# Optimization experiments

Hardware: AMD Instinct MI355X
Metric: run time of the kernel (lower is better)

## Reference

```python
import jax, jax.numpy as jnp
import numpy as np


def setup_inputs() -> dict:
    key = jax.random.key(0)
    k1, k2, k3, k4 = jax.random.split(key, 4)
    n_nodes, n_edges, d_in, d_half = 100000, 1600000, 256, 128
    x = jax.random.normal(k1, (n_nodes, d_in), dtype=jnp.float32)
    edge_index = jax.random.randint(k2, (2, n_edges), 0, n_nodes, dtype=jnp.int64)
    W_f = jax.random.normal(k3, (d_half, d_in), dtype=jnp.float32) * (1.0 / np.sqrt(d_in))
    W_b = jax.random.normal(k4, (d_half, d_in), dtype=jnp.float32) * (1.0 / np.sqrt(d_in))
    bias_param = jnp.zeros((2 * d_half,), dtype=jnp.float32)
    return {"x": x, "edge_index": edge_index, "W_f": W_f, "W_b": W_b, "bias_param": bias_param}


def _inv_sqrt(deg):
    # deg.pow(-0.5) with inf -> 0
    return jnp.where(deg > 0, jax.lax.rsqrt(deg), 0.0)


def reference(x, edge_index, W_f, W_b, bias_param):
    n_nodes = x.shape[0]
    # add_remaining_self_loops with fill value 1
    loops = jnp.arange(n_nodes, dtype=edge_index.dtype)
    ei = jnp.concatenate([edge_index, jnp.stack([loops, loops])], axis=1)
    n_e = ei.shape[1]
    w = jnp.ones((n_e,), dtype=x.dtype)
    # directed_norm, flow='source_to_target': col, row = edge_index
    col, row = ei[0], ei[1]
    in_deg = jax.ops.segment_sum(w, col, num_segments=n_nodes)
    out_deg = jax.ops.segment_sum(w, row, num_segments=n_nodes)
    ew = _inv_sqrt(out_deg)[row] * w * _inv_sqrt(in_deg)[col]  # [E]
    # adj_forward: source=row, target=col ; adj_backward: source=col, target=row
    mf = (x @ W_f.T)[row] * ew[:, None]           # [E, d_half]
    y_forward = jax.ops.segment_sum(mf, col, num_segments=n_nodes)
    mb = (x @ W_b.T)[col] * ew[:, None]           # [E, d_half]
    y_backward = jax.ops.segment_sum(mb, row, num_segments=n_nodes)
    y = jnp.concatenate([y_forward, y_backward], axis=-1) + bias_param
    return y
```

## Files before the change

### kernel.cpp

```cpp
#include <hip/hip_runtime.h>

#define D_IN 256
#define D_HALF 128

typedef __attribute__((ext_vector_type(8))) short short8;
typedef __attribute__((ext_vector_type(4))) float float4v;

__device__ __forceinline__ unsigned short f2bf(float f) {
    union { float f; unsigned u; } v; v.f = f;
    unsigned r = v.u + 0x7FFF + ((v.u >> 16) & 1);
    return (unsigned short)(r >> 16);
}
__device__ __forceinline__ float bflo(unsigned u) { union { unsigned u; float f; } v; v.u = u << 16; return v.f; }
__device__ __forceinline__ float bfhi(unsigned u) { union { unsigned u; float f; } v; v.u = u & 0xffff0000u; return v.f; }

__device__ __forceinline__ void async16(const void* g, void* l) {
    __builtin_amdgcn_global_load_lds(
        (const __attribute__((address_space(1))) unsigned int*)g,
        (__attribute__((address_space(3))) unsigned int*)l, 16, 0, 0);
}


#define S_SH 9
#define NBK_MAX 512
#define CAP 12288
#define EPB 4096

__global__ void zero_kernel(int* __restrict__ gcnt) {
    int i = blockIdx.x * blockDim.x + threadIdx.x;
    if (i < NBK_MAX) gcnt[i] = 0;
}

__global__ void p1_kernel(const int* __restrict__ col, const int* __restrict__ row,
                          int* __restrict__ gcnt, unsigned* __restrict__ staging,
                          int N, int E) {
    __shared__ int hist[NBK_MAX];
    __shared__ int base_[NBK_MAX];
    const int tid = threadIdx.x;
    hist[tid] = 0; hist[tid + 256] = 0;
    __syncthreads();

    int ce[16], re[16], rf_[16], rb_[16];
    const int e0 = blockIdx.x * EPB;
    #pragma unroll
    for (int j = 0; j < 16; ++j) {
        int e = e0 + j * 256 + tid;
        if (e < E) {
            ce[j] = col[e];
            re[j] = row[e];
            rf_[j] = atomicAdd(&hist[ce[j] >> S_SH], 1);
            rb_[j] = atomicAdd(&hist[(N + re[j]) >> S_SH], 1);
        } else {
            ce[j] = -1; re[j] = 0; rf_[j] = 0; rb_[j] = 0;
        }
    }
    __syncthreads();

    #pragma unroll
    for (int b = 0; b < NBK_MAX / 256; ++b) {
        int idx = b * 256 + tid;
        int c = hist[idx];
        if (c) base_[idx] = idx * CAP + atomicAdd(&gcnt[idx], c);
    }
    __syncthreads();

    #pragma unroll
    for (int j = 0; j < 16; ++j) {
        if (ce[j] >= 0) {
            int c = ce[j], r = re[j];
            staging[(size_t)base_[c >> S_SH] + rf_[j]] =
                ((unsigned)(c & 511) << 23) | (unsigned)r;
            int sb = N + r;
            staging[(size_t)base_[sb >> S_SH] + rb_[j]] =
                ((unsigned)(sb & 511) << 23) | (unsigned)c;
        }
    }
}

__global__ void scanB_kernel(const int* __restrict__ gcnt, int* __restrict__ bbase, int nbuck) {
    __shared__ int s[NBK_MAX];
    const int tid = threadIdx.x;
    int v = (tid < nbuck) ? gcnt[tid] : 0;
    s[tid] = v;
    __syncthreads();
    for (int d = 1; d < NBK_MAX; d <<= 1) {
        int t = (tid >= d) ? s[tid - d] : 0;
        __syncthreads();
        s[tid] += t;
        __syncthreads();
    }
    if (tid < nbuck) bbase[tid] = s[tid] - v;
}

__global__ void bsort_kernel(const unsigned* __restrict__ staging, const int* __restrict__ gcnt,
                             const int* __restrict__ bbase, int* __restrict__ cnt,
                             int* __restrict__ offs, int* __restrict__ adj, int M) {
    __shared__ int lcnt[NBK_MAX];
    __shared__ int s[256];
    __shared__ int lbuf[CAP];
    const int tid = threadIdx.x;
    const int b = blockIdx.x;
    const int s0 = b << S_SH;
    lcnt[tid] = 0; lcnt[tid + 256] = 0;
    __syncthreads();

    const int count = gcnt[b];
    const int base = bbase[b];
    const unsigned* __restrict__ st = staging + (size_t)b * CAP;

    for (int i = tid; i < count; i += 256)
        atomicAdd(&lcnt[st[i] >> 23], 1);
    __syncthreads();

    int v0 = lcnt[2 * tid], v1 = lcnt[2 * tid + 1];
    int pair = v0 + v1;
    s[tid] = pair;
    __syncthreads();
    for (int d = 1; d < 256; d <<= 1) {
        int t = (tid >= d) ? s[tid - d] : 0;
        __syncthreads();
        s[tid] += t;
        __syncthreads();
    }
    int excl = s[tid] - pair;

    int gs0 = s0 + 2 * tid;
    if (gs0 < M)     { cnt[gs0] = v0;     offs[gs0] = base + excl; }
    if (gs0 + 1 < M) { cnt[gs0 + 1] = v1; offs[gs0 + 1] = base + excl + v0; }

    lcnt[2 * tid] = excl;
    lcnt[2 * tid + 1] = excl + v0;
    __syncthreads();

    for (int i = tid; i < count; i += 256) {
        unsigned it = st[i];
        int sl = it >> 23;
        int p = atomicAdd(&lcnt[sl], 1);
        lbuf[p] = (int)(it & 0x7fffffu);
    }
    __syncthreads();
    for (int i = tid; i < count; i += 256)
        adj[base + i] = lbuf[i];
}

__global__ void inv_kernel(const int* __restrict__ cnt,
                           float* __restrict__ inv_in, float* __restrict__ inv_out, int N) {
    int i = blockIdx.x * blockDim.x + threadIdx.x;
    if (i < N) {
        inv_in[i]  = rsqrtf((float)(cnt[i] + 1));
        inv_out[i] = rsqrtf((float)(cnt[N + i] + 1));
    }
}


__global__ void cast_kernel(const float* __restrict__ x, const float* __restrict__ Wf,
                            const float* __restrict__ Wb, unsigned short* __restrict__ xb,
                            unsigned short* __restrict__ wcat, int n4) {
    int i = blockIdx.x * blockDim.x + threadIdx.x;
    const int w4 = (2 * D_HALF * D_IN) / 4;
    if (i < n4) {
        float4 v = ((const float4*)x)[i];
        ushort4 o = { f2bf(v.x), f2bf(v.y), f2bf(v.z), f2bf(v.w) };
        ((ushort4*)xb)[i] = o;
    } else if (i < n4 + w4) {
        int j = i - n4;
        int elem = j * 4;
        const float* src = (elem < D_HALF * D_IN) ? (Wf + elem) : (Wb + (elem - D_HALF * D_IN));
        float4 v = *(const float4*)src;
        ushort4 o = { f2bf(v.x), f2bf(v.y), f2bf(v.z), f2bf(v.w) };
        ((ushort4*)wcat)[j] = o;
    }
}


#define BM 128
#define BN 128
#define BK 32

__global__ void gemm_mfma_kernel(const unsigned short* __restrict__ xb,
                                 const unsigned short* __restrict__ wcat,
                                 const float* __restrict__ inv_in,
                                 const float* __restrict__ inv_out,
                                 unsigned short* __restrict__ zb, int N) {
    __shared__ __align__(16) unsigned short As[BM * BK];
    __shared__ __align__(16) unsigned short Bs[BN * BK];
    const int tid = threadIdx.x;
    const int wave = tid >> 6;
    const int lane = tid & 63;
    const int bm = blockIdx.x * BM;
    const int bn = blockIdx.y * BN;
    const int warpM = wave >> 1;
    const int warpN = wave & 1;
    const int l15 = lane & 15;
    const int quad = lane >> 4;

    float4v acc[4][4];
    #pragma unroll
    for (int i = 0; i < 4; ++i)
        #pragma unroll
        for (int j = 0; j < 4; ++j)
            acc[i][j] = (float4v){0.f, 0.f, 0.f, 0.f};

    for (int kt = 0; kt < D_IN / BK; ++kt) {
        #pragma unroll
        for (int iss = 0; iss < 2; ++iss) {
            const int pbase = iss * 256 + wave * 64;
            const int p = pbase + lane;
            const int m = p >> 2;
            const int g = (p & 3) ^ ((m >> 1) & 3);
            int gm = bm + m; if (gm >= N) gm = N - 1;
            async16(xb + (size_t)gm * D_IN + kt * BK + g * 8, &As[pbase * 8]);
            async16(wcat + (size_t)(bn + m) * D_IN + kt * BK + g * 8, &Bs[pbase * 8]);
        }
        __syncthreads();

        short8 af[4], bfr[4];
        #pragma unroll
        for (int mi = 0; mi < 4; ++mi) {
            int m = warpM * 64 + mi * 16 + l15;
            af[mi] = *(const short8*)&As[m * BK + (quad ^ ((m >> 1) & 3)) * 8];
        }
        #pragma unroll
        for (int ni = 0; ni < 4; ++ni) {
            int n = warpN * 64 + ni * 16 + l15;
            bfr[ni] = *(const short8*)&Bs[n * BK + (quad ^ ((n >> 1) & 3)) * 8];
        }
        #pragma unroll
        for (int mi = 0; mi < 4; ++mi)
            #pragma unroll
            for (int ni = 0; ni < 4; ++ni)
                acc[mi][ni] = __builtin_amdgcn_mfma_f32_16x16x32_bf16(af[mi], bfr[ni], acc[mi][ni], 0, 0, 0);
        __syncthreads();
    }

    const float* __restrict__ sc = (blockIdx.y == 0) ? inv_out : inv_in;
    #pragma unroll
    for (int mi = 0; mi < 4; ++mi) {
        #pragma unroll
        for (int reg = 0; reg < 4; ++reg) {
            int gm = bm + warpM * 64 + mi * 16 + quad * 4 + reg;
            if (gm < N) {
                float s = sc[gm];
                #pragma unroll
                for (int ni = 0; ni < 4; ++ni) {
                    int gn = bn + warpN * 64 + ni * 16 + l15;
                    zb[(size_t)gm * D_IN + gn] = f2bf(acc[mi][ni][reg] * s);
                }
            }
        }
    }
}


__global__ void gather_kernel(const unsigned short* __restrict__ zb, const int* __restrict__ adj,
                              const int* __restrict__ offs, const int* __restrict__ cnt,
                              const float* __restrict__ inv_in, const float* __restrict__ inv_out,
                              const float* __restrict__ bias,
                              float* __restrict__ out, int N) {
    const int wave = threadIdx.x >> 6;
    const int lane = threadIdx.x & 63;
    const int slot = blockIdx.x * 4 + wave;
    if (slot >= 2 * N) return;
    const int dir = (slot >= N) ? 1 : 0;
    const int node = slot - dir * N;
    const int csr = slot;
    const int beg = offs[csr];
    const int deg = cnt[csr];
    const int end = beg + deg;
    const int g4 = lane >> 4;
    const int l15 = lane & 15;
    const int chu = dir * D_HALF + 8 * l15;
    const int pa = g4 << 2;

    float a0 = 0.f, a1 = 0.f, a2 = 0.f, a3 = 0.f;
    float a4 = 0.f, a5 = 0.f, a6 = 0.f, a7 = 0.f;

    for (int base = beg; base < end; base += 64) {
        int len = end - base; if (len > 64) len = 64;
        int nb = (lane < len) ? adj[base + lane] : node;
        #pragma unroll 8
        for (int j0 = 0; j0 < len; j0 += 4) {
            int nsel = __builtin_amdgcn_ds_bpermute((j0 << 2) + pa, nb);
            float m = (j0 + g4 < len) ? 1.0f : 0.0f;
            const uint4 u = *(const uint4*)&zb[(size_t)nsel * D_IN + chu];
            a0 = fmaf(m, bflo(u.x), a0); a1 = fmaf(m, bfhi(u.x), a1);
            a2 = fmaf(m, bflo(u.y), a2); a3 = fmaf(m, bfhi(u.y), a3);
            a4 = fmaf(m, bflo(u.z), a4); a5 = fmaf(m, bfhi(u.z), a5);
            a6 = fmaf(m, bflo(u.w), a6); a7 = fmaf(m, bfhi(u.w), a7);
        }
    }

    a0 += __shfl_xor(a0, 16); a0 += __shfl_xor(a0, 32);
    a1 += __shfl_xor(a1, 16); a1 += __shfl_xor(a1, 32);
    a2 += __shfl_xor(a2, 16); a2 += __shfl_xor(a2, 32);
    a3 += __shfl_xor(a3, 16); a3 += __shfl_xor(a3, 32);
    a4 += __shfl_xor(a4, 16); a4 += __shfl_xor(a4, 32);
    a5 += __shfl_xor(a5, 16); a5 += __shfl_xor(a5, 32);
    a6 += __shfl_xor(a6, 16); a6 += __shfl_xor(a6, 32);
    a7 += __shfl_xor(a7, 16); a7 += __shfl_xor(a7, 32);

    if (g4 == 0) {
        const uint4 us = *(const uint4*)&zb[(size_t)node * D_IN + chu];
        a0 += bflo(us.x); a1 += bfhi(us.x);
        a2 += bflo(us.y); a3 += bfhi(us.y);
        a4 += bflo(us.z); a5 += bfhi(us.z);
        a6 += bflo(us.w); a7 += bfhi(us.w);

        const float scale = dir ? inv_out[node] : inv_in[node];
        const float4 bv0 = *(const float4*)&bias[chu];
        const float4 bv1 = *(const float4*)&bias[chu + 4];
        size_t oi = (size_t)node * D_IN + chu;
        float4 o0 = { bv0.x + scale * a0, bv0.y + scale * a1,
                      bv0.z + scale * a2, bv0.w + scale * a3 };
        float4 o1 = { bv1.x + scale * a4, bv1.y + scale * a5,
                      bv1.z + scale * a6, bv1.w + scale * a7 };
        *(float4*)&out[oi] = o0;
        *(float4*)&out[oi + 4] = o1;
    }
}


extern "C" void kernel_launch(void* const* d_in, const int* in_sizes, int n_in,
                              void* d_out, int out_size, void* d_ws, size_t ws_size,
                              hipStream_t stream) {
    const float* x    = (const float*)d_in[0];
    const int*   ei   = (const int*)d_in[1];
    const float* Wf   = (const float*)d_in[2];
    const float* Wb   = (const float*)d_in[3];
    const float* bias = (const float*)d_in[4];
    float* out = (float*)d_out;

    const int N = in_sizes[0] / D_IN;
    const int E = in_sizes[1] / 2;
    const int* col = ei;
    const int* rowp = ei + E;

    char* ws = (char*)d_ws;
    unsigned short* xb = (unsigned short*)ws;   ws += (size_t)N * D_IN * sizeof(short);
    unsigned short* zb = (unsigned short*)ws;   ws += (size_t)N * D_IN * sizeof(short);
    unsigned short* wcat = (unsigned short*)ws; ws += (size_t)2 * D_HALF * D_IN * sizeof(short);
    int* cnt = (int*)ws;            ws += (size_t)2 * N * sizeof(int);
    int* offs = (int*)ws;           ws += (size_t)2 * N * sizeof(int);
    float* inv_in = (float*)ws;     ws += (size_t)N * sizeof(float);
    float* inv_out = (float*)ws;    ws += (size_t)N * sizeof(float);
    int* adj = (int*)ws;            ws += (size_t)2 * E * sizeof(int);
    int* gcnt = (int*)ws;           ws += NBK_MAX * sizeof(int);
    int* bbase = (int*)ws;          ws += NBK_MAX * sizeof(int);

    unsigned* staging = (unsigned*)zb;

    const int M = 2 * N;
    const int nbuck = (M + 511) >> S_SH;

    const int n4 = N * D_IN / 4;
    const int w4 = (2 * D_HALF * D_IN) / 4;
    cast_kernel<<<(n4 + w4 + 255) / 256, 256, 0, stream>>>(x, Wf, Wb, xb, wcat, n4);

    zero_kernel<<<2, 256, 0, stream>>>(gcnt);
    p1_kernel<<<(E + EPB - 1) / EPB, 256, 0, stream>>>(col, rowp, gcnt, staging, N, E);
    scanB_kernel<<<1, NBK_MAX, 0, stream>>>(gcnt, bbase, nbuck);
    bsort_kernel<<<nbuck, 256, 0, stream>>>(staging, gcnt, bbase, cnt, offs, adj, M);
    inv_kernel<<<(N + 255) / 256, 256, 0, stream>>>(cnt, inv_in, inv_out, N);

    dim3 ggrid((N + BM - 1) / BM, D_IN / BN);
    gemm_mfma_kernel<<<ggrid, 256, 0, stream>>>(xb, wcat, inv_in, inv_out, zb, N);

    gather_kernel<<<(2 * N + 3) / 4, 256, 0, stream>>>(zb, adj, offs, cnt, inv_in, inv_out, bias, out, N);
}
```

Measured before the change: 394.9 us.

## Fuse cast into edge-bucketing kernel and fold scan and rsqrt into bucket sort

The bf16 cast of x and weights now runs as extra blocks of the edge-bucketing kernel, so the two independent jobs share one launch and can overlap. The global bucket-offset scan moves into every bucket-sort block, each of which redundantly scans all bucket counts. The inverse-sqrt degree computation is also done inside the bucket sort. This removes three launches and their serialization at the cost of redundant per-block scan work. gcnt is read for indices up to 511, which is fine since zero_kernel clears all 512 entries.

```diff
diff --git a/kernel.cpp b/kernel.cpp
--- a/kernel.cpp
+++ b/kernel.cpp
@@ -31,12 +31,34 @@
     if (i < NBK_MAX) gcnt[i] = 0;
 }
 
-__global__ void p1_kernel(const int* __restrict__ col, const int* __restrict__ row,
-                          int* __restrict__ gcnt, unsigned* __restrict__ staging,
-                          int N, int E) {
+__global__ void p1_cast_kernel(const int* __restrict__ col, const int* __restrict__ row,
+                               int* __restrict__ gcnt, unsigned* __restrict__ staging,
+                               int N, int E, int nP1,
+                               const float* __restrict__ x, const float* __restrict__ Wf,
+                               const float* __restrict__ Wb, unsigned short* __restrict__ xb,
+                               unsigned short* __restrict__ wcat, int n4) {
     __shared__ int hist[NBK_MAX];
     __shared__ int base_[NBK_MAX];
     const int tid = threadIdx.x;
+
+    if (blockIdx.x >= nP1) {
+        int i = (blockIdx.x - nP1) * 256 + tid;
+        const int w4 = (2 * D_HALF * D_IN) / 4;
+        if (i < n4) {
+            float4 v = ((const float4*)x)[i];
+            ushort4 o = { f2bf(v.x), f2bf(v.y), f2bf(v.z), f2bf(v.w) };
+            ((ushort4*)xb)[i] = o;
+        } else if (i < n4 + w4) {
+            int j = i - n4;
+            int elem = j * 4;
+            const float* src = (elem < D_HALF * D_IN) ? (Wf + elem) : (Wb + (elem - D_HALF * D_IN));
+            float4 v = *(const float4*)src;
+            ushort4 o = { f2bf(v.x), f2bf(v.y), f2bf(v.z), f2bf(v.w) };
+            ((ushort4*)wcat)[j] = o;
+        }
+        return;
+    }
+
     hist[tid] = 0; hist[tid + 256] = 0;
     __syncthreads();
 
@@ -77,35 +99,38 @@
     }
 }
 
-__global__ void scanB_kernel(const int* __restrict__ gcnt, int* __restrict__ bbase, int nbuck) {
-    __shared__ int s[NBK_MAX];
-    const int tid = threadIdx.x;
-    int v = (tid < nbuck) ? gcnt[tid] : 0;
-    s[tid] = v;
-    __syncthreads();
-    for (int d = 1; d < NBK_MAX; d <<= 1) {
-        int t = (tid >= d) ? s[tid - d] : 0;
-        __syncthreads();
-        s[tid] += t;
-        __syncthreads();
-    }
-    if (tid < nbuck) bbase[tid] = s[tid] - v;
-}
-
 __global__ void bsort_kernel(const unsigned* __restrict__ staging, const int* __restrict__ gcnt,
-                             const int* __restrict__ bbase, int* __restrict__ cnt,
-                             int* __restrict__ offs, int* __restrict__ adj, int M) {
+                             int* __restrict__ cnt, int* __restrict__ offs,
+                             float* __restrict__ inv_in, float* __restrict__ inv_out,
+                             int* __restrict__ adj, int N, int M) {
     __shared__ int lcnt[NBK_MAX];
     __shared__ int s[256];
     __shared__ int lbuf[CAP];
+    __shared__ int bc[2];
     const int tid = threadIdx.x;
     const int b = blockIdx.x;
     const int s0 = b << S_SH;
+
+    int g0 = gcnt[2 * tid], g1 = gcnt[2 * tid + 1];
+    int pairB = g0 + g1;
+    s[tid] = pairB;
+    __syncthreads();
+    for (int d = 1; d < 256; d <<= 1) {
+        int t = (tid >= d) ? s[tid - d] : 0;
+        __syncthreads();
+        s[tid] += t;
+        __syncthreads();
+    }
+    if (tid == (b >> 1)) {
+        int excl = s[tid] - pairB;
+        bc[0] = excl + ((b & 1) ? g0 : 0);
+        bc[1] = (b & 1) ? g1 : g0;
+    }
     lcnt[tid] = 0; lcnt[tid + 256] = 0;
     __syncthreads();
 
-    const int count = gcnt[b];
-    const int base = bbase[b];
+    const int base = bc[0];
+    const int count = bc[1];
     const unsigned* __restrict__ st = staging + (size_t)b * CAP;
 
     for (int i = tid; i < count; i += 256)
@@ -125,8 +150,16 @@
     int excl = s[tid] - pair;
 
     int gs0 = s0 + 2 * tid;
-    if (gs0 < M)     { cnt[gs0] = v0;     offs[gs0] = base + excl; }
-    if (gs0 + 1 < M) { cnt[gs0 + 1] = v1; offs[gs0 + 1] = base + excl + v0; }
+    if (gs0 < M) {
+        cnt[gs0] = v0;  offs[gs0] = base + excl;
+        if (gs0 < N) inv_in[gs0] = rsqrtf((float)(v0 + 1));
+        else         inv_out[gs0 - N] = rsqrtf((float)(v0 + 1));
+    }
+    if (gs0 + 1 < M) {
+        cnt[gs0 + 1] = v1;  offs[gs0 + 1] = base + excl + v0;
+        if (gs0 + 1 < N) inv_in[gs0 + 1] = rsqrtf((float)(v1 + 1));
+        else             inv_out[gs0 + 1 - N] = rsqrtf((float)(v1 + 1));
+    }
 
     lcnt[2 * tid] = excl;
     lcnt[2 * tid + 1] = excl + v0;
@@ -141,35 +174,6 @@
     __syncthreads();
     for (int i = tid; i < count; i += 256)
         adj[base + i] = lbuf[i];
-}
-
-__global__ void inv_kernel(const int* __restrict__ cnt,
-                           float* __restrict__ inv_in, float* __restrict__ inv_out, int N) {
-    int i = blockIdx.x * blockDim.x + threadIdx.x;
-    if (i < N) {
-        inv_in[i]  = rsqrtf((float)(cnt[i] + 1));
-        inv_out[i] = rsqrtf((float)(cnt[N + i] + 1));
-    }
-}
-
-
-__global__ void cast_kernel(const float* __restrict__ x, const float* __restrict__ Wf,
-                            const float* __restrict__ Wb, unsigned short* __restrict__ xb,
-                            unsigned short* __restrict__ wcat, int n4) {
-    int i = blockIdx.x * blockDim.x + threadIdx.x;
-    const int w4 = (2 * D_HALF * D_IN) / 4;
-    if (i < n4) {
-        float4 v = ((const float4*)x)[i];
-        ushort4 o = { f2bf(v.x), f2bf(v.y), f2bf(v.z), f2bf(v.w) };
-        ((ushort4*)xb)[i] = o;
-    } else if (i < n4 + w4) {
-        int j = i - n4;
-        int elem = j * 4;
-        const float* src = (elem < D_HALF * D_IN) ? (Wf + elem) : (Wb + (elem - D_HALF * D_IN));
-        float4 v = *(const float4*)src;
-        ushort4 o = { f2bf(v.x), f2bf(v.y), f2bf(v.z), f2bf(v.w) };
-        ((ushort4*)wcat)[j] = o;
-    }
 }
 
 
@@ -345,22 +349,20 @@
     float* inv_out = (float*)ws;    ws += (size_t)N * sizeof(float);
     int* adj = (int*)ws;            ws += (size_t)2 * E * sizeof(int);
     int* gcnt = (int*)ws;           ws += NBK_MAX * sizeof(int);
-    int* bbase = (int*)ws;          ws += NBK_MAX * sizeof(int);
 
     unsigned* staging = (unsigned*)zb;
 
     const int M = 2 * N;
     const int nbuck = (M + 511) >> S_SH;
-
+    const int nP1 = (E + EPB - 1) / EPB;
     const int n4 = N * D_IN / 4;
     const int w4 = (2 * D_HALF * D_IN) / 4;
-    cast_kernel<<<(n4 + w4 + 255) / 256, 256, 0, stream>>>(x, Wf, Wb, xb, wcat, n4);
+    const int nCast = (n4 + w4 + 255) / 256;
 
     zero_kernel<<<2, 256, 0, stream>>>(gcnt);
-    p1_kernel<<<(E + EPB - 1) / EPB, 256, 0, stream>>>(col, rowp, gcnt, staging, N, E);
-    scanB_kernel<<<1, NBK_MAX, 0, stream>>>(gcnt, bbase, nbuck);
-    bsort_kernel<<<nbuck, 256, 0, stream>>>(staging, gcnt, bbase, cnt, offs, adj, M);
-    inv_kernel<<<(N + 255) / 256, 256, 0, stream>>>(cnt, inv_in, inv_out, N);
+    p1_cast_kernel<<<nP1 + nCast, 256, 0, stream>>>(col, rowp, gcnt, staging, N, E, nP1,
+                                                    x, Wf, Wb, xb, wcat, n4);
+    bsort_kernel<<<nbuck, 256, 0, stream>>>(staging, gcnt, cnt, offs, inv_in, inv_out, adj, N, M);
 
     dim3 ggrid((N + BM - 1) / BM, D_IN / BN);
     gemm_mfma_kernel<<<ggrid, 256, 0, stream>>>(xb, wcat, inv_in, inv_out, zb, N);
```

New measurement: 380.6 us. -3.6%, faster.
